# Optimization experiments

Measured on AMD Instinct MI355X. Metric: run time of the kernel, lower is better.

Reference implementation:

```python
import jax, jax.numpy as jnp
import numpy as np

N = 100000
E = 400000
H = 128
GROUPS = 4
K = 5
GC = H // GROUPS
RMS_EPS = 1.1920929e-07  # torch uses finfo(float32).eps when eps=None


def setup_inputs() -> dict:
    key = jax.random.key(0)
    k1, k2, k3, k4, k5 = jax.random.split(key, 5)
    x = jax.random.normal(k1, (N, H), dtype=jnp.float32)
    edge_index = jax.random.randint(k2, (2, E), 0, N, dtype=jnp.int64)
    edge_weight_norm = jax.random.uniform(k3, (E,), dtype=jnp.float32)
    # parameters
    cheb_coeffs = jax.random.uniform(k4, (GROUPS, K + 1), dtype=jnp.float32,
                                     minval=-0.1, maxval=0.1)  # xavier-ish, gain 0.1
    group_scale = jnp.ones((GROUPS,), dtype=jnp.float32)
    group_bias = jnp.zeros((GROUPS,), dtype=jnp.float32)
    rms_weight = jnp.ones((H,), dtype=jnp.float32)
    return {
        "x": x,
        "edge_weight_norm": edge_weight_norm,
        "cheb_coeffs": cheb_coeffs,
        "group_scale": group_scale,
        "group_bias": group_bias,
        "rms_weight": rms_weight,
        "edge_index": edge_index,
    }


def _propagate(h, src, dst, ew):
    # gather-mul-scatter: out[dst] += h[src] * ew
    msg = h[src] * ew[:, None]            # [E, H]
    return jax.ops.segment_sum(msg, dst, num_segments=N)


def reference(x, edge_weight_norm, cheb_coeffs, group_scale, group_bias,
              rms_weight, edge_index):
    src, dst = edge_index[0], edge_index[1]
    ew = edge_weight_norm.astype(x.dtype)

    def gexpand(c):  # [GROUPS] -> broadcast over [N, GROUPS, GC]
        return c[None, :, None]

    xg = x.reshape(N, GROUPS, GC)
    result = gexpand(cheb_coeffs[:, 0]) * xg  # T0 term

    # K >= 1: Chebyshev recurrence T_k = 2*A T_{k-1} - T_{k-2}
    T_prev2 = x
    T_prev1 = _propagate(x, src, dst, ew)
    result = result + gexpand(cheb_coeffs[:, 1]) * T_prev1.reshape(N, GROUPS, GC)

    def step(carry, coeff_k):
        T_p1, T_p2, res = carry
        T_curr = 2.0 * _propagate(T_p1, src, dst, ew) - T_p2
        res = res + coeff_k[None, :, None] * T_curr.reshape(N, GROUPS, GC)
        return (T_curr, T_p1, res), None

    coeffs_rest = cheb_coeffs[:, 2:].T  # [K-1, GROUPS]
    (T_prev1, T_prev2, result), _ = jax.lax.scan(
        step, (T_prev1, T_prev2, result), coeffs_rest)

    result = result * gexpand(group_scale) + gexpand(group_bias)
    out = result.reshape(N, H)
    # RMSNorm (affine) then SiLU; dropout is identity in eval
    rms = jax.lax.rsqrt(jnp.mean(out * out, axis=-1, keepdims=True) + RMS_EPS)
    out = out * rms * rms_weight
    return jax.nn.silu(out)
```

## Files before the change

kernel.cpp:

```cpp
#include <hip/hip_runtime.h>
#include <hip/hip_fp16.h>
#include <math.h>

#define N_NODES 100000
#define N_EDGES 400000
#define HDIM    128
#define KP1     6
#define RMS_EPS 1.1920929e-07f

#define SCAN_B  256
#define N_SCAN_BLOCKS ((N_NODES + SCAN_B - 1) / SCAN_B)

__global__ __launch_bounds__(256)
void x2h_kernel(const float* __restrict__ x, __half* __restrict__ xh) {
    size_t i = (size_t)blockIdx.x * blockDim.x + threadIdx.x;
    const size_t total = (size_t)N_NODES * HDIM / 8;
    if (i >= total) return;
    const float4 a = reinterpret_cast<const float4*>(x)[2 * i];
    const float4 b = reinterpret_cast<const float4*>(x)[2 * i + 1];
    int4 r;
    __half2* h = reinterpret_cast<__half2*>(&r);
    h[0] = __floats2half2_rn(a.x, a.y);
    h[1] = __floats2half2_rn(a.z, a.w);
    h[2] = __floats2half2_rn(b.x, b.y);
    h[3] = __floats2half2_rn(b.z, b.w);
    reinterpret_cast<int4*>(xh)[i] = r;
}

__global__ void hist_kernel(const int* __restrict__ dst, int* __restrict__ deg) {
    int e = blockIdx.x * blockDim.x + threadIdx.x;
    if (e >= N_EDGES) return;
    atomicAdd(&deg[dst[e]], 1);
}

__global__ void scan_local_kernel(const int* __restrict__ deg,
                                  int* __restrict__ inc,
                                  int* __restrict__ blockSums) {
    __shared__ int lds[SCAN_B];
    int i = blockIdx.x * SCAN_B + threadIdx.x;
    int v = (i < N_NODES) ? deg[i] : 0;
    lds[threadIdx.x] = v;
    __syncthreads();
    #pragma unroll
    for (int off = 1; off < SCAN_B; off <<= 1) {
        int t = (threadIdx.x >= off) ? lds[threadIdx.x - off] : 0;
        __syncthreads();
        lds[threadIdx.x] += t;
        __syncthreads();
    }
    if (i < N_NODES) inc[i] = lds[threadIdx.x];
    if (threadIdx.x == SCAN_B - 1) blockSums[blockIdx.x] = lds[SCAN_B - 1];
}

__global__ void scan_blocks_kernel(int* __restrict__ blockSums) {
    __shared__ int lds[512];
    int v = (threadIdx.x < N_SCAN_BLOCKS) ? blockSums[threadIdx.x] : 0;
    lds[threadIdx.x] = v;
    __syncthreads();
    #pragma unroll
    for (int off = 1; off < 512; off <<= 1) {
        int t = ((int)threadIdx.x >= off) ? lds[threadIdx.x - off] : 0;
        __syncthreads();
        lds[threadIdx.x] += t;
        __syncthreads();
    }
    if (threadIdx.x < N_SCAN_BLOCKS)
        blockSums[threadIdx.x] = (threadIdx.x == 0) ? 0 : lds[threadIdx.x - 1];
}

__global__ void finalize_kernel(const int* __restrict__ deg,
                                const int* __restrict__ inc,
                                const int* __restrict__ blockSums,
                                int* __restrict__ rowptr,
                                int* __restrict__ cursor) {
    int i = blockIdx.x * SCAN_B + threadIdx.x;
    if (i >= N_NODES) return;
    int ex = inc[i] - deg[i] + blockSums[i >> 8];
    rowptr[i] = ex;
    cursor[i] = ex;
    if (i == 0) rowptr[N_NODES] = N_EDGES;
}

__global__ void fill_kernel(const int* __restrict__ src,
                            const int* __restrict__ dst,
                            const float* __restrict__ ew,
                            int* __restrict__ cursor,
                            int2* __restrict__ epack) {
    int e = blockIdx.x * blockDim.x + threadIdx.x;
    if (e >= N_EDGES) return;
    int d = dst[e];
    int pos = atomicAdd(&cursor[d], 1);
    int2 p;
    p.x = src[e] * HDIM;
    p.y = __float_as_int(ew[e]);
    epack[pos] = p;
}

__device__ __forceinline__ void fma8_h(const __half* __restrict__ p, float w, float* S) {
    int4 r = *reinterpret_cast<const int4*>(p);
    const __half2* h = reinterpret_cast<const __half2*>(&r);
    #pragma unroll
    for (int q = 0; q < 4; ++q) {
        float2 f = __half22float2(h[q]);
        S[2 * q + 0] += w * f.x;
        S[2 * q + 1] += w * f.y;
    }
}
__device__ __forceinline__ void load8_h(const __half* __restrict__ p, float* o) {
    int4 r = *reinterpret_cast<const int4*>(p);
    const __half2* h = reinterpret_cast<const __half2*>(&r);
    #pragma unroll
    for (int q = 0; q < 4; ++q) {
        float2 f = __half22float2(h[q]);
        o[2 * q + 0] = f.x;
        o[2 * q + 1] = f.y;
    }
}
__device__ __forceinline__ void store8_h(__half* __restrict__ p, const float* v) {
    int4 r;
    __half2* h = reinterpret_cast<__half2*>(&r);
    #pragma unroll
    for (int q = 0; q < 4; ++q)
        h[q] = __floats2half2_rn(v[2 * q + 0], v[2 * q + 1]);
    *reinterpret_cast<int4*>(p) = r;
}

template <int MODE>
__global__ __launch_bounds__(256)
void prop_kernel(const __half* __restrict__ Tp1h,
                 const __half* __restrict__ Tp2h,
                 const __half* __restrict__ xh,
                 const int* __restrict__ rowptr,
                 const int2* __restrict__ epack,
                 const float* __restrict__ cheb,
                 __half* __restrict__ Tch,
                 const __half* __restrict__ T1h,
                 const __half* __restrict__ T2h,
                 float* __restrict__ out,
                 const float* __restrict__ gscale,
                 const float* __restrict__ gbias,
                 const float* __restrict__ rmsw) {
    int grp = threadIdx.x >> 4;
    int sub = threadIdx.x & 15;
    int row = blockIdx.x * 16 + grp;
    if (row >= N_NODES) return;

    int beg = rowptr[row];
    int end = rowptr[row + 1];
    int d8 = sub * 8;

    float S[8] = {0, 0, 0, 0, 0, 0, 0, 0};
    int j = beg;
    for (; j + 3 < end; j += 4) {
        int2 e0 = epack[j], e1 = epack[j + 1], e2 = epack[j + 2], e3 = epack[j + 3];
        float w0 = __int_as_float(e0.y), w1 = __int_as_float(e1.y);
        float w2 = __int_as_float(e2.y), w3 = __int_as_float(e3.y);
        fma8_h(Tp1h + e0.x + d8, w0, S);
        fma8_h(Tp1h + e1.x + d8, w1, S);
        fma8_h(Tp1h + e2.x + d8, w2, S);
        fma8_h(Tp1h + e3.x + d8, w3, S);
    }
    for (; j < end; ++j) {
        int2 e0 = epack[j];
        float w = __int_as_float(e0.y);
        fma8_h(Tp1h + e0.x + d8, w, S);
    }

    size_t off = (size_t)row * HDIM + d8;
    int g = sub >> 2;

    if (MODE == 0) {
        store8_h(Tch + off, S);
    } else if (MODE == 1) {
        float p[8];
        load8_h(Tp2h + off, p);
        float t[8];
        #pragma unroll
        for (int q = 0; q < 8; ++q) t[q] = 2.0f * S[q] - p[q];
        store8_h(Tch + off, t);
    } else {
        float t3[8], t1[8], t2[8], t4[8], xr[8];
        load8_h(Tp2h + off, t3);
        load8_h(T1h + off, t1);
        load8_h(T2h + off, t2);
        load8_h(Tp1h + off, t4);
        load8_h(xh + off, xr);

        float c0 = cheb[g * KP1 + 0], c1 = cheb[g * KP1 + 1], c2 = cheb[g * KP1 + 2];
        float c3 = cheb[g * KP1 + 3], c4 = cheb[g * KP1 + 4], c5 = cheb[g * KP1 + 5];
        float sc = gscale[g];
        float bi = gbias[g];

        float o[8];
        float ss = 0.0f;
        #pragma unroll
        for (int q = 0; q < 8; ++q) {
            float t5 = 2.0f * S[q] - t3[q];
            float v = c0 * xr[q] + c1 * t1[q] + c2 * t2[q] + c3 * t3[q]
                    + c4 * t4[q] + c5 * t5;
            v = v * sc + bi;
            o[q] = v;
            ss += v * v;
        }
        #pragma unroll
        for (int m = 1; m < 16; m <<= 1)
            ss += __shfl_xor(ss, m, 64);
        float r = rsqrtf(ss * (1.0f / HDIM) + RMS_EPS);

        float4 wa = *reinterpret_cast<const float4*>(rmsw + d8);
        float4 wb = *reinterpret_cast<const float4*>(rmsw + d8 + 4);
        float wv[8] = {wa.x, wa.y, wa.z, wa.w, wb.x, wb.y, wb.z, wb.w};
        float res[8];
        #pragma unroll
        for (int q = 0; q < 8; ++q) {
            float a = o[q] * r * wv[q];
            res[q] = a / (1.0f + expf(-a));
        }
        float4 ra = {res[0], res[1], res[2], res[3]};
        float4 rb = {res[4], res[5], res[6], res[7]};
        *reinterpret_cast<float4*>(out + off) = ra;
        *reinterpret_cast<float4*>(out + off + 4) = rb;
    }
}

extern "C" void kernel_launch(void* const* d_in, const int* in_sizes, int n_in,
                              void* d_out, int out_size, void* d_ws, size_t ws_size,
                              hipStream_t stream) {
    const float* x      = (const float*)d_in[0];
    const float* ew     = (const float*)d_in[1];
    const float* cheb   = (const float*)d_in[2];
    const float* gscale = (const float*)d_in[3];
    const float* gbias  = (const float*)d_in[4];
    const float* rmsw   = (const float*)d_in[5];
    const int*   eidx   = (const int*)d_in[6];
    const int*   src    = eidx;
    const int*   dst    = eidx + N_EDGES;
    float* out = (float*)d_out;

    const size_t NH = (size_t)N_NODES * HDIM;
    __half* xh  = (__half*)d_ws;
    __half* T1  = xh + NH;
    __half* T2  = T1 + NH;
    __half* T3  = T2 + NH;
    __half* T4  = T3 + NH;
    int2*  epack    = (int2*)(T4 + NH);
    int*   deg      = (int*)(epack + N_EDGES);
    int*   inc      = deg + N_NODES;
    int*   rowptr   = inc + N_NODES;
    int*   cursor   = rowptr + N_NODES + 1;
    int*   blockSums= cursor + N_NODES;

    const int TB = 256;
    const int edge_blocks = (N_EDGES + TB - 1) / TB;
    const int conv_blocks = (int)((NH / 8 + TB - 1) / TB);
    const int prop_blocks = (N_NODES + 15) / 16;

    x2h_kernel<<<conv_blocks, TB, 0, stream>>>(x, xh);
    hipMemsetAsync(deg, 0, N_NODES * sizeof(int), stream);
    hist_kernel<<<edge_blocks, TB, 0, stream>>>(dst, deg);
    scan_local_kernel<<<N_SCAN_BLOCKS, SCAN_B, 0, stream>>>(deg, inc, blockSums);
    scan_blocks_kernel<<<1, 512, 0, stream>>>(blockSums);
    finalize_kernel<<<N_SCAN_BLOCKS, SCAN_B, 0, stream>>>(deg, inc, blockSums, rowptr, cursor);
    fill_kernel<<<edge_blocks, TB, 0, stream>>>(src, dst, ew, cursor, epack);

    prop_kernel<0><<<prop_blocks, TB, 0, stream>>>(xh, nullptr, nullptr, rowptr, epack,
                                                   cheb, T1, nullptr, nullptr,
                                                   out, gscale, gbias, rmsw);
    prop_kernel<1><<<prop_blocks, TB, 0, stream>>>(T1, xh, nullptr, rowptr, epack,
                                                   cheb, T2, nullptr, nullptr,
                                                   out, gscale, gbias, rmsw);
    prop_kernel<1><<<prop_blocks, TB, 0, stream>>>(T2, T1, nullptr, rowptr, epack,
                                                   cheb, T3, nullptr, nullptr,
                                                   out, gscale, gbias, rmsw);
    prop_kernel<1><<<prop_blocks, TB, 0, stream>>>(T3, T2, nullptr, rowptr, epack,
                                                   cheb, T4, nullptr, nullptr,
                                                   out, gscale, gbias, rmsw);
    prop_kernel<2><<<prop_blocks, TB, 0, stream>>>(T4, T3, xh, rowptr, epack,
                                                   cheb, nullptr, T1, T2,
                                                   out, gscale, gbias, rmsw);
}
```

Before: 201.7 us.

## Slice features into 16-wide planes, pack edges into one word, split normalization

Features are now stored in eight slice-major planes of 16 halves per node. Each thread handles one node for one slice, so the gathered working set per slice (about 3.2MB) can stay in cache. Each edge is compressed into a single 32-bit word holding the source index plus a 15-bit quantized weight, which halves edge traffic but loses weight precision. The final step writes pre-norm values over xh along with per-slice sums of squares, and a separate norm kernel applies RMSNorm and SiLU. Nontemporal loads and stores are added for the streaming accesses.

After: 347.0 us. 72.0% more time.

```diff
diff --git a/kernel.cpp b/kernel.cpp
--- a/kernel.cpp
+++ b/kernel.cpp
@@ -5,26 +5,34 @@
 #define N_NODES 100000
 #define N_EDGES 400000
 #define HDIM    128
+#define NSLICE  8
+#define SDIM    16
 #define KP1     6
 #define RMS_EPS 1.1920929e-07f
 
 #define SCAN_B  256
 #define N_SCAN_BLOCKS ((N_NODES + SCAN_B - 1) / SCAN_B)
 
+typedef int intx4 __attribute__((ext_vector_type(4)));
+
+#define SS ((size_t)N_NODES * SDIM)
+
 __global__ __launch_bounds__(256)
-void x2h_kernel(const float* __restrict__ x, __half* __restrict__ xh) {
-    size_t i = (size_t)blockIdx.x * blockDim.x + threadIdx.x;
-    const size_t total = (size_t)N_NODES * HDIM / 8;
-    if (i >= total) return;
-    const float4 a = reinterpret_cast<const float4*>(x)[2 * i];
-    const float4 b = reinterpret_cast<const float4*>(x)[2 * i + 1];
+void x2h_slice_kernel(const float* __restrict__ x, __half* __restrict__ xh) {
+    int t = blockIdx.x * 256 + threadIdx.x;
+    int n = t >> 4;
+    int l = t & 15;
+    if (n >= N_NODES) return;
+    int s = l >> 1, h = l & 1;
+    const float4* px = reinterpret_cast<const float4*>(x + (size_t)n * HDIM + l * 8);
+    float4 a = px[0], b = px[1];
     int4 r;
-    __half2* h = reinterpret_cast<__half2*>(&r);
-    h[0] = __floats2half2_rn(a.x, a.y);
-    h[1] = __floats2half2_rn(a.z, a.w);
-    h[2] = __floats2half2_rn(b.x, b.y);
-    h[3] = __floats2half2_rn(b.z, b.w);
-    reinterpret_cast<int4*>(xh)[i] = r;
+    __half2* hh = reinterpret_cast<__half2*>(&r);
+    hh[0] = __floats2half2_rn(a.x, a.y);
+    hh[1] = __floats2half2_rn(a.z, a.w);
+    hh[2] = __floats2half2_rn(b.x, b.y);
+    hh[3] = __floats2half2_rn(b.z, b.w);
+    *reinterpret_cast<int4*>(xh + (size_t)s * SS + (size_t)n * SDIM + h * 8) = r;
 }
 
 __global__ void hist_kernel(const int* __restrict__ dst, int* __restrict__ deg) {
@@ -85,116 +93,142 @@
                             const int* __restrict__ dst,
                             const float* __restrict__ ew,
                             int* __restrict__ cursor,
-                            int2* __restrict__ epack) {
+                            int* __restrict__ epk) {
     int e = blockIdx.x * blockDim.x + threadIdx.x;
     if (e >= N_EDGES) return;
     int d = dst[e];
     int pos = atomicAdd(&cursor[d], 1);
-    int2 p;
-    p.x = src[e] * HDIM;
-    p.y = __float_as_int(ew[e]);
-    epack[pos] = p;
-}
-
-__device__ __forceinline__ void fma8_h(const __half* __restrict__ p, float w, float* S) {
-    int4 r = *reinterpret_cast<const int4*>(p);
-    const __half2* h = reinterpret_cast<const __half2*>(&r);
-    #pragma unroll
-    for (int q = 0; q < 4; ++q) {
-        float2 f = __half22float2(h[q]);
-        S[2 * q + 0] += w * f.x;
-        S[2 * q + 1] += w * f.y;
-    }
-}
-__device__ __forceinline__ void load8_h(const __half* __restrict__ p, float* o) {
-    int4 r = *reinterpret_cast<const int4*>(p);
-    const __half2* h = reinterpret_cast<const __half2*>(&r);
-    #pragma unroll
-    for (int q = 0; q < 4; ++q) {
-        float2 f = __half22float2(h[q]);
-        o[2 * q + 0] = f.x;
-        o[2 * q + 1] = f.y;
-    }
-}
-__device__ __forceinline__ void store8_h(__half* __restrict__ p, const float* v) {
-    int4 r;
-    __half2* h = reinterpret_cast<__half2*>(&r);
-    #pragma unroll
-    for (int q = 0; q < 4; ++q)
-        h[q] = __floats2half2_rn(v[2 * q + 0], v[2 * q + 1]);
-    *reinterpret_cast<int4*>(p) = r;
+    int wf = (int)(ew[e] * 32768.0f);
+    if (wf > 32767) wf = 32767;
+    if (wf < 0) wf = 0;
+    unsigned p = ((unsigned)src[e] << 15) | (unsigned)wf;
+    epk[pos] = (int)p;
+}
+
+__device__ __forceinline__ void gfma(const __half* sb, int p, float* S) {
+    int m = ((unsigned)p) >> 15;
+    float w = (float)(p & 32767) * (1.0f / 32768.0f);
+    const int4* q = reinterpret_cast<const int4*>(sb + (size_t)m * SDIM);
+    int4 a = q[0];
+    int4 b = q[1];
+    const __half2* ha = reinterpret_cast<const __half2*>(&a);
+    const __half2* hb = reinterpret_cast<const __half2*>(&b);
+    #pragma unroll
+    for (int d = 0; d < 4; ++d) {
+        float2 f = __half22float2(ha[d]);
+        S[2 * d]     += w * f.x;
+        S[2 * d + 1] += w * f.y;
+    }
+    #pragma unroll
+    for (int d = 0; d < 4; ++d) {
+        float2 f = __half22float2(hb[d]);
+        S[8 + 2 * d]     += w * f.x;
+        S[8 + 2 * d + 1] += w * f.y;
+    }
+}
+__device__ __forceinline__ void ntload16(const __half* p, float* o) {
+    intx4 a = __builtin_nontemporal_load(reinterpret_cast<const intx4*>(p));
+    intx4 b = __builtin_nontemporal_load(reinterpret_cast<const intx4*>(p) + 1);
+    union { intx4 v; __half2 h[4]; } ua, ub;
+    ua.v = a; ub.v = b;
+    #pragma unroll
+    for (int d = 0; d < 4; ++d) {
+        float2 f = __half22float2(ua.h[d]);
+        o[2 * d]     = f.x;
+        o[2 * d + 1] = f.y;
+    }
+    #pragma unroll
+    for (int d = 0; d < 4; ++d) {
+        float2 f = __half22float2(ub.h[d]);
+        o[8 + 2 * d]     = f.x;
+        o[8 + 2 * d + 1] = f.y;
+    }
+}
+__device__ __forceinline__ void store16(__half* p, const float* v) {
+    int4 r0, r1;
+    __half2* h0 = reinterpret_cast<__half2*>(&r0);
+    __half2* h1 = reinterpret_cast<__half2*>(&r1);
+    #pragma unroll
+    for (int d = 0; d < 4; ++d) h0[d] = __floats2half2_rn(v[2 * d], v[2 * d + 1]);
+    #pragma unroll
+    for (int d = 0; d < 4; ++d) h1[d] = __floats2half2_rn(v[8 + 2 * d], v[8 + 2 * d + 1]);
+    reinterpret_cast<int4*>(p)[0] = r0;
+    reinterpret_cast<int4*>(p)[1] = r1;
+}
+__device__ __forceinline__ void ntstore16(__half* p, const float* v) {
+    union { intx4 v; __half2 h[4]; } r0, r1;
+    #pragma unroll
+    for (int d = 0; d < 4; ++d) r0.h[d] = __floats2half2_rn(v[2 * d], v[2 * d + 1]);
+    #pragma unroll
+    for (int d = 0; d < 4; ++d) r1.h[d] = __floats2half2_rn(v[8 + 2 * d], v[8 + 2 * d + 1]);
+    __builtin_nontemporal_store(r0.v, reinterpret_cast<intx4*>(p));
+    __builtin_nontemporal_store(r1.v, reinterpret_cast<intx4*>(p) + 1);
 }
 
 template <int MODE>
 __global__ __launch_bounds__(256)
-void prop_kernel(const __half* __restrict__ Tp1h,
-                 const __half* __restrict__ Tp2h,
-                 const __half* __restrict__ xh,
-                 const int* __restrict__ rowptr,
-                 const int2* __restrict__ epack,
-                 const float* __restrict__ cheb,
-                 __half* __restrict__ Tch,
-                 const __half* __restrict__ T1h,
-                 const __half* __restrict__ T2h,
-                 float* __restrict__ out,
-                 const float* __restrict__ gscale,
-                 const float* __restrict__ gbias,
-                 const float* __restrict__ rmsw) {
-    int grp = threadIdx.x >> 4;
-    int sub = threadIdx.x & 15;
-    int row = blockIdx.x * 16 + grp;
-    if (row >= N_NODES) return;
-
-    int beg = rowptr[row];
-    int end = rowptr[row + 1];
-    int d8 = sub * 8;
-
-    float S[8] = {0, 0, 0, 0, 0, 0, 0, 0};
+void prop_slice(const __half* __restrict__ Tsrc,
+                const __half* __restrict__ Tp2,
+                const __half* xh,
+                const __half* __restrict__ T1b,
+                const __half* __restrict__ T2b,
+                const int* __restrict__ rowptr,
+                const int* __restrict__ epk,
+                const float* __restrict__ cheb,
+                const float* __restrict__ gscale,
+                const float* __restrict__ gbias,
+                __half* Tc,
+                float* __restrict__ ssqp) {
+    int slice = blockIdx.x & 7;
+    int n = (blockIdx.x >> 3) * 256 + threadIdx.x;
+    if (n >= N_NODES) return;
+    const __half* sb = Tsrc + (size_t)slice * SS;
+    int beg = rowptr[n];
+    int end = rowptr[n + 1];
+
+    float S[16];
+    #pragma unroll
+    for (int q = 0; q < 16; ++q) S[q] = 0.0f;
+
     int j = beg;
-    for (; j + 3 < end; j += 4) {
-        int2 e0 = epack[j], e1 = epack[j + 1], e2 = epack[j + 2], e3 = epack[j + 3];
-        float w0 = __int_as_float(e0.y), w1 = __int_as_float(e1.y);
-        float w2 = __int_as_float(e2.y), w3 = __int_as_float(e3.y);
-        fma8_h(Tp1h + e0.x + d8, w0, S);
-        fma8_h(Tp1h + e1.x + d8, w1, S);
-        fma8_h(Tp1h + e2.x + d8, w2, S);
-        fma8_h(Tp1h + e3.x + d8, w3, S);
-    }
-    for (; j < end; ++j) {
-        int2 e0 = epack[j];
-        float w = __int_as_float(e0.y);
-        fma8_h(Tp1h + e0.x + d8, w, S);
-    }
-
-    size_t off = (size_t)row * HDIM + d8;
-    int g = sub >> 2;
+    for (; j + 1 < end; j += 2) {
+        int p0 = __builtin_nontemporal_load(epk + j);
+        int p1 = __builtin_nontemporal_load(epk + j + 1);
+        gfma(sb, p0, S);
+        gfma(sb, p1, S);
+    }
+    if (j < end) {
+        int p0 = __builtin_nontemporal_load(epk + j);
+        gfma(sb, p0, S);
+    }
+
+    size_t off = (size_t)slice * SS + (size_t)n * SDIM;
 
     if (MODE == 0) {
-        store8_h(Tch + off, S);
+        store16(Tc + off, S);
     } else if (MODE == 1) {
-        float p[8];
-        load8_h(Tp2h + off, p);
-        float t[8];
+        float p[16];
+        ntload16(Tp2 + off, p);
+        float t[16];
         #pragma unroll
-        for (int q = 0; q < 8; ++q) t[q] = 2.0f * S[q] - p[q];
-        store8_h(Tch + off, t);
+        for (int q = 0; q < 16; ++q) t[q] = 2.0f * S[q] - p[q];
+        store16(Tc + off, t);
     } else {
-        float t3[8], t1[8], t2[8], t4[8], xr[8];
-        load8_h(Tp2h + off, t3);
-        load8_h(T1h + off, t1);
-        load8_h(T2h + off, t2);
-        load8_h(Tp1h + off, t4);
-        load8_h(xh + off, xr);
-
+        float t3[16], xr[16], t1[16], t2[16], t4[16];
+        ntload16(Tp2 + off, t3);
+        ntload16(xh + off, xr);
+        ntload16(T1b + off, t1);
+        ntload16(T2b + off, t2);
+        ntload16(Tsrc + off, t4);
+        int g = slice >> 1;
         float c0 = cheb[g * KP1 + 0], c1 = cheb[g * KP1 + 1], c2 = cheb[g * KP1 + 2];
         float c3 = cheb[g * KP1 + 3], c4 = cheb[g * KP1 + 4], c5 = cheb[g * KP1 + 5];
         float sc = gscale[g];
         float bi = gbias[g];
-
-        float o[8];
+        float o[16];
         float ss = 0.0f;
         #pragma unroll
-        for (int q = 0; q < 8; ++q) {
+        for (int q = 0; q < 16; ++q) {
             float t5 = 2.0f * S[q] - t3[q];
             float v = c0 * xr[q] + c1 * t1[q] + c2 * t2[q] + c3 * t3[q]
                     + c4 * t4[q] + c5 * t5;
@@ -202,25 +236,51 @@
             o[q] = v;
             ss += v * v;
         }
-        #pragma unroll
-        for (int m = 1; m < 16; m <<= 1)
-            ss += __shfl_xor(ss, m, 64);
-        float r = rsqrtf(ss * (1.0f / HDIM) + RMS_EPS);
-
-        float4 wa = *reinterpret_cast<const float4*>(rmsw + d8);
-        float4 wb = *reinterpret_cast<const float4*>(rmsw + d8 + 4);
-        float wv[8] = {wa.x, wa.y, wa.z, wa.w, wb.x, wb.y, wb.z, wb.w};
-        float res[8];
-        #pragma unroll
-        for (int q = 0; q < 8; ++q) {
-            float a = o[q] * r * wv[q];
-            res[q] = a / (1.0f + expf(-a));
-        }
-        float4 ra = {res[0], res[1], res[2], res[3]};
-        float4 rb = {res[4], res[5], res[6], res[7]};
-        *reinterpret_cast<float4*>(out + off) = ra;
-        *reinterpret_cast<float4*>(out + off + 4) = rb;
-    }
+        ntstore16(Tc + off, o);
+        ssqp[slice * N_NODES + n] = ss;
+    }
+}
+
+__global__ __launch_bounds__(256)
+void norm_kernel(const __half* __restrict__ oh,
+                 const float* __restrict__ ssqp,
+                 const float* __restrict__ rmsw,
+                 float* __restrict__ out) {
+    int t = blockIdx.x * 256 + threadIdx.x;
+    int n = t >> 4;
+    int l = t & 15;
+    if (n >= N_NODES) return;
+    int s = l >> 1, h = l & 1;
+    size_t off = (size_t)s * SS + (size_t)n * SDIM + h * 8;
+    int4 r = *reinterpret_cast<const int4*>(oh + off);
+    const __half2* hh = reinterpret_cast<const __half2*>(&r);
+    float o[8];
+    #pragma unroll
+    for (int d = 0; d < 4; ++d) {
+        float2 f = __half22float2(hh[d]);
+        o[2 * d]     = f.x;
+        o[2 * d + 1] = f.y;
+    }
+    float ss = ssqp[s * N_NODES + n];
+    ss += __shfl_xor(ss, 2, 64);
+    ss += __shfl_xor(ss, 4, 64);
+    ss += __shfl_xor(ss, 8, 64);
+    float rr = rsqrtf(ss * (1.0f / HDIM) + RMS_EPS);
+    int dbase = l * 8;
+    float4 wa = *reinterpret_cast<const float4*>(rmsw + dbase);
+    float4 wb = *reinterpret_cast<const float4*>(rmsw + dbase + 4);
+    float wv[8] = {wa.x, wa.y, wa.z, wa.w, wb.x, wb.y, wb.z, wb.w};
+    float res[8];
+    #pragma unroll
+    for (int q = 0; q < 8; ++q) {
+        float a = o[q] * rr * wv[q];
+        res[q] = a / (1.0f + expf(-a));
+    }
+    float4 ra = {res[0], res[1], res[2], res[3]};
+    float4 rb = {res[4], res[5], res[6], res[7]};
+    float* op = out + (size_t)n * HDIM + dbase;
+    *reinterpret_cast<float4*>(op) = ra;
+    *reinterpret_cast<float4*>(op + 4) = rb;
 }
 
 extern "C" void kernel_launch(void* const* d_in, const int* in_sizes, int n_in,
@@ -238,13 +298,14 @@
     float* out = (float*)d_out;
 
     const size_t NH = (size_t)N_NODES * HDIM;
-    __half* xh  = (__half*)d_ws;
-    __half* T1  = xh + NH;
-    __half* T2  = T1 + NH;
-    __half* T3  = T2 + NH;
-    __half* T4  = T3 + NH;
-    int2*  epack    = (int2*)(T4 + NH);
-    int*   deg      = (int*)(epack + N_EDGES);
+    __half* xh = (__half*)d_ws;
+    __half* T1 = xh + NH;
+    __half* T2 = T1 + NH;
+    __half* T3 = T2 + NH;
+    __half* T4 = T3 + NH;
+    int*   epk      = (int*)(T4 + NH);
+    float* ssqp     = (float*)(epk + N_EDGES);
+    int*   deg      = (int*)(ssqp + NSLICE * N_NODES);
     int*   inc      = deg + N_NODES;
     int*   rowptr   = inc + N_NODES;
     int*   cursor   = rowptr + N_NODES + 1;
@@ -252,30 +313,31 @@
 
     const int TB = 256;
     const int edge_blocks = (N_EDGES + TB - 1) / TB;
-    const int conv_blocks = (int)((NH / 8 + TB - 1) / TB);
-    const int prop_blocks = (N_NODES + 15) / 16;
-
-    x2h_kernel<<<conv_blocks, TB, 0, stream>>>(x, xh);
+    const int lane_blocks = (N_NODES * 16 + TB - 1) / TB;
+    const int prop_blocks = NSLICE * ((N_NODES + TB - 1) / TB);
+
+    x2h_slice_kernel<<<lane_blocks, TB, 0, stream>>>(x, xh);
     hipMemsetAsync(deg, 0, N_NODES * sizeof(int), stream);
     hist_kernel<<<edge_blocks, TB, 0, stream>>>(dst, deg);
     scan_local_kernel<<<N_SCAN_BLOCKS, SCAN_B, 0, stream>>>(deg, inc, blockSums);
     scan_blocks_kernel<<<1, 512, 0, stream>>>(blockSums);
     finalize_kernel<<<N_SCAN_BLOCKS, SCAN_B, 0, stream>>>(deg, inc, blockSums, rowptr, cursor);
-    fill_kernel<<<edge_blocks, TB, 0, stream>>>(src, dst, ew, cursor, epack);
-
-    prop_kernel<0><<<prop_blocks, TB, 0, stream>>>(xh, nullptr, nullptr, rowptr, epack,
-                                                   cheb, T1, nullptr, nullptr,
-                                                   out, gscale, gbias, rmsw);
-    prop_kernel<1><<<prop_blocks, TB, 0, stream>>>(T1, xh, nullptr, rowptr, epack,
-                                                   cheb, T2, nullptr, nullptr,
-                                                   out, gscale, gbias, rmsw);
-    prop_kernel<1><<<prop_blocks, TB, 0, stream>>>(T2, T1, nullptr, rowptr, epack,
-                                                   cheb, T3, nullptr, nullptr,
-                                                   out, gscale, gbias, rmsw);
-    prop_kernel<1><<<prop_blocks, TB, 0, stream>>>(T3, T2, nullptr, rowptr, epack,
-                                                   cheb, T4, nullptr, nullptr,
-                                                   out, gscale, gbias, rmsw);
-    prop_kernel<2><<<prop_blocks, TB, 0, stream>>>(T4, T3, xh, rowptr, epack,
-                                                   cheb, nullptr, T1, T2,
-                                                   out, gscale, gbias, rmsw);
-}
+    fill_kernel<<<edge_blocks, TB, 0, stream>>>(src, dst, ew, cursor, epk);
+
+    prop_slice<0><<<prop_blocks, TB, 0, stream>>>(xh, nullptr, nullptr, nullptr, nullptr,
+                                                  rowptr, epk, cheb, gscale, gbias,
+                                                  T1, nullptr);
+    prop_slice<1><<<prop_blocks, TB, 0, stream>>>(T1, xh, nullptr, nullptr, nullptr,
+                                                  rowptr, epk, cheb, gscale, gbias,
+                                                  T2, nullptr);
+    prop_slice<1><<<prop_blocks, TB, 0, stream>>>(T2, T1, nullptr, nullptr, nullptr,
+                                                  rowptr, epk, cheb, gscale, gbias,
+                                                  T3, nullptr);
+    prop_slice<1><<<prop_blocks, TB, 0, stream>>>(T3, T2, nullptr, nullptr, nullptr,
+                                                  rowptr, epk, cheb, gscale, gbias,
+                                                  T4, nullptr);
+    prop_slice<2><<<prop_blocks, TB, 0, stream>>>(T4, T3, xh, T1, T2,
+                                                  rowptr, epk, cheb, gscale, gbias,
+                                                  xh, ssqp);
+    norm_kernel<<<lane_blocks, TB, 0, stream>>>(xh, ssqp, rmsw, out);
+}
```
